# Performance work log

Measured on AMD Instinct MI355X. Metric: run time of the kernel, lower is better.

## Reference

```python
import jax, jax.numpy as jnp
import numpy as np

N, L, D = 256, 512, 512


def _attention(x, W_in, W_out, apply_tanh):
    # x: [N, L, D]; 'general' attention: project query, score against context (=x)
    q = jnp.einsum('bld,ed->ble', x, W_in)          # [N, L, D]
    scores = jnp.einsum('bld,bmd->blm', q, x)       # [N, L, L]
    w = jax.nn.softmax(scores, axis=-1)             # softmax over keys
    mix = jnp.einsum('blm,bmd->bld', w, x)          # [N, L, D]
    comb = jnp.concatenate([mix, q], axis=-1)       # [N, L, 2D]
    out = jnp.einsum('blc,dc->bld', comb, W_out)    # Linear(2D, D), no bias
    return jnp.tanh(out) if apply_tanh else out


def setup_inputs() -> dict:
    key = jax.random.key(0)
    k1, k2, k3, k4, k5 = jax.random.split(key, 5)
    s = 0.02
    return {
        'embeddings': jax.random.normal(k1, (N, L, D), dtype=jnp.float32),
        'W_in1': jax.random.normal(k2, (D, D), dtype=jnp.float32) * s,
        'W_out1': jax.random.normal(k3, (D, 2 * D), dtype=jnp.float32) * s,
        'W_in2': jax.random.normal(k4, (D, D), dtype=jnp.float32) * s,
        'W_out2': jax.random.normal(k5, (D, 2 * D), dtype=jnp.float32) * s,
    }


def reference(embeddings, W_in1, W_out1, W_in2, W_out2):
    x = _attention(embeddings, W_in1, W_out1, apply_tanh=True)   # block 1 (tanh)
    x = _attention(x, W_in2, W_out2, apply_tanh=False)           # block 2 (no tanh)
    # transpose(1,2) + avg_pool1d over full length == mean over L
    pooled = jnp.mean(x, axis=1)                                  # [N, D]
    return pooled.reshape(pooled.shape[0], -1, 1, 1)              # [N, D, 1, 1]
```

## Files before the change

### kernel.cpp

```cpp
#include <hip/hip_runtime.h>
#include <cstdint>
#include <cstddef>

typedef uint16_t u16;
typedef __attribute__((ext_vector_type(8))) short bf16x8;
typedef __attribute__((ext_vector_type(4))) float f32x4;
typedef __attribute__((ext_vector_type(4))) uint16_t u16x4;

#define GLOBAL_AS(p) (const __attribute__((address_space(1))) void*)(p)
#define LDS_AS(p)    (__attribute__((address_space(3))) void*)(p)

__device__ __forceinline__ void wait_all_bar(){
  asm volatile("s_waitcnt vmcnt(0) lgkmcnt(0)" ::: "memory");
  __builtin_amdgcn_s_barrier();
  asm volatile("" ::: "memory");
}
__device__ __forceinline__ void wait_lgkm_bar(){
  asm volatile("s_waitcnt lgkmcnt(0)" ::: "memory");
  __builtin_amdgcn_s_barrier();
  asm volatile("" ::: "memory");
}

__device__ __forceinline__ u16 f2b(float f){
  uint32_t u = __float_as_uint(f);
  u += 0x7fff + ((u >> 16) & 1);
  return (u16)(u >> 16);
}
__device__ __forceinline__ float b2f(u16 h){
  return __uint_as_float(((uint32_t)h) << 16);
}

__global__ void cvt_bf16_kernel(const float* __restrict__ src, u16* __restrict__ dst, int n){
  int i = (blockIdx.x * 256 + threadIdx.x) * 4;
  if (i >= n) return;
  float4 f = *(const float4*)(src + i);
  u16x4 o; o.x = f2b(f.x); o.y = f2b(f.y); o.z = f2b(f.z); o.w = f2b(f.w);
  *(u16x4*)(dst + i) = o;
}

__global__ void cvtT_kernel(const float* __restrict__ src, u16* __restrict__ x, u16* __restrict__ xT){
  __shared__ u16 tile[64][68];
  size_t b = blockIdx.y;
  int t = blockIdx.x;
  int r0 = (t >> 3) * 64, c0 = (t & 7) * 64;
  const float* s = src + b * 262144;
  u16* dx = x + b * 262144;
  u16* dT = xT + b * 262144;
  int tx = threadIdx.x & 63, ty = threadIdx.x >> 6;
  #pragma unroll
  for (int k = 0; k < 16; k++){
    int r = ty * 16 + k;
    u16 v = f2b(s[(size_t)(r0 + r) * 512 + c0 + tx]);
    dx[(size_t)(r0 + r) * 512 + c0 + tx] = v;
    tile[r][tx] = v;
  }
  __syncthreads();
  #pragma unroll
  for (int k = 0; k < 16; k++){
    int c = ty * 16 + k;
    dT[(size_t)(c0 + c) * 512 + r0 + tx] = tile[tx][c];
  }
}

__global__ void transpose512_kernel(const u16* __restrict__ src, u16* __restrict__ dst){
  __shared__ u16 tile[64][68];
  size_t b = blockIdx.y;
  int t = blockIdx.x;
  int r0 = (t >> 3) * 64, c0 = (t & 7) * 64;
  const u16* s = src + b * 262144;
  u16* d = dst + b * 262144;
  int tx = threadIdx.x & 63, ty = threadIdx.x >> 6;
  #pragma unroll
  for (int k = 0; k < 16; k++){
    int r = ty * 16 + k;
    tile[r][tx] = s[(size_t)(r0 + r) * 512 + c0 + tx];
  }
  __syncthreads();
  #pragma unroll
  for (int k = 0; k < 16; k++){
    int c = ty * 16 + k;
    d[(size_t)(c0 + c) * 512 + r0 + tx] = tile[tx][c];
  }
}

__global__ __launch_bounds__(512, 2) void attn_kernel(
    const u16* __restrict__ q, const u16* __restrict__ x, const u16* __restrict__ xT,
    u16* __restrict__ mix, int batPerXcd)
{
  __shared__ __align__(16) u16 U[64 * 520];
  __shared__ __align__(16) u16 Bx[2][512 * 32];
  __shared__ float stats[2][64][8];
  const int64_t E = 262144;
  int id = blockIdx.x;
  int tile = (id >> 3) & 7;
  int64_t bat = (int64_t)(id & 7) * batPerXcd + (id >> 6);
  q += bat * E; x += bat * E; xT += bat * E; mix += bat * E;
  int m0 = tile * 64;
  int tid = threadIdx.x, lane = tid & 63, w = tid >> 6;
  int fr = lane & 15, qd = lane >> 4, fq = qd * 8;

  auto stage = [&](const u16* __restrict__ src, int buf, int k0){
    #pragma unroll
    for (int s = 0; s < 4; s++){
      const u16* g = src + (size_t)(s * 128 + (tid >> 2)) * 512 + k0 + (tid & 3) * 8;
      __builtin_amdgcn_global_load_lds(GLOBAL_AS(g), LDS_AS(&Bx[buf][s * 4096 + tid * 8]), 16, 0, 0);
    }
  };

  stage(x, 0, 0);

  #pragma unroll
  for (int c = 0; c < 8; c++){
    int id2 = c * 512 + tid;
    int row = id2 >> 6, cb = id2 & 63;
    *(bf16x8*)&U[row * 520 + cb * 8] =
        *(const bf16x8*)(q + (size_t)(m0 + row) * 512 + cb * 8);
  }

  f32x4 acc[4][4];
  #pragma unroll
  for (int i = 0; i < 4; i++)
    #pragma unroll
    for (int j = 0; j < 4; j++) acc[i][j] = (f32x4){0.f, 0.f, 0.f, 0.f};

  wait_all_bar();

  for (int it = 0; it < 16; ++it){
    if (it < 15) stage(x, (it + 1) & 1, (it + 1) * 32);
    int k0 = it * 32;
    bf16x8 af[4], bfr[4];
    #pragma unroll
    for (int i = 0; i < 4; i++) af[i]  = *(const bf16x8*)&U[(i * 16 + fr) * 520 + k0 + fq];
    #pragma unroll
    for (int j = 0; j < 4; j++) bfr[j] = *(const bf16x8*)&Bx[it & 1][(w * 64 + j * 16 + fr) * 32 + fq];
    #pragma unroll
    for (int i = 0; i < 4; i++)
      #pragma unroll
      for (int j = 0; j < 4; j++)
        acc[i][j] = __builtin_amdgcn_mfma_f32_16x16x32_bf16(af[i], bfr[j], acc[i][j], 0, 0, 0);
    wait_all_bar();
  }

  stage(xT, 0, 0);

  float inv[4][4];
  #pragma unroll
  for (int i = 0; i < 4; i++)
    #pragma unroll
    for (int r = 0; r < 4; r++){
      float m = acc[i][0][r];
      #pragma unroll
      for (int j = 1; j < 4; j++) m = fmaxf(m, acc[i][j][r]);
      #pragma unroll
      for (int o = 1; o <= 8; o <<= 1) m = fmaxf(m, __shfl_xor(m, o));
      if (fr == 0) stats[0][i * 16 + qd * 4 + r][w] = m;
    }
  wait_lgkm_bar();
  #pragma unroll
  for (int i = 0; i < 4; i++)
    #pragma unroll
    for (int r = 0; r < 4; r++){
      int row = i * 16 + qd * 4 + r;
      float m = stats[0][row][0];
      #pragma unroll
      for (int t = 1; t < 8; t++) m = fmaxf(m, stats[0][row][t]);
      float s = 0.f;
      #pragma unroll
      for (int j = 0; j < 4; j++){
        float e = __expf(acc[i][j][r] - m);
        acc[i][j][r] = e; s += e;
      }
      #pragma unroll
      for (int o = 1; o <= 8; o <<= 1) s += __shfl_xor(s, o);
      if (fr == 0) stats[1][row][w] = s;
    }
  wait_lgkm_bar();
  #pragma unroll
  for (int i = 0; i < 4; i++)
    #pragma unroll
    for (int r = 0; r < 4; r++){
      int row = i * 16 + qd * 4 + r;
      float s = stats[1][row][0];
      #pragma unroll
      for (int t = 1; t < 8; t++) s += stats[1][row][t];
      inv[i][r] = 1.0f / s;
    }
  #pragma unroll
  for (int i = 0; i < 4; i++)
    #pragma unroll
    for (int r = 0; r < 4; r++)
      #pragma unroll
      for (int j = 0; j < 4; j++){
        int row = i * 16 + qd * 4 + r;
        int col = w * 64 + j * 16 + fr;
        uint32_t mine = f2b(acc[i][j][r] * inv[i][r]);
        uint32_t oth = (uint32_t)__shfl_xor((int)mine, 1);
        if (!(fr & 1)) *(uint32_t*)&U[row * 520 + col] = mine | (oth << 16);
      }
  wait_all_bar();

  #pragma unroll
  for (int i = 0; i < 4; i++)
    #pragma unroll
    for (int j = 0; j < 4; j++) acc[i][j] = (f32x4){0.f, 0.f, 0.f, 0.f};
  for (int it = 0; it < 16; ++it){
    if (it < 15) stage(xT, (it + 1) & 1, (it + 1) * 32);
    int k0 = it * 32;
    bf16x8 af[4], bfr[4];
    #pragma unroll
    for (int i = 0; i < 4; i++) af[i]  = *(const bf16x8*)&U[(i * 16 + fr) * 520 + k0 + fq];
    #pragma unroll
    for (int j = 0; j < 4; j++) bfr[j] = *(const bf16x8*)&Bx[it & 1][(w * 64 + j * 16 + fr) * 32 + fq];
    #pragma unroll
    for (int i = 0; i < 4; i++)
      #pragma unroll
      for (int j = 0; j < 4; j++)
        acc[i][j] = __builtin_amdgcn_mfma_f32_16x16x32_bf16(af[i], bfr[j], acc[i][j], 0, 0, 0);
    wait_all_bar();
  }
  #pragma unroll
  for (int i = 0; i < 4; i++)
    #pragma unroll
    for (int j = 0; j < 4; j++)
      #pragma unroll
      for (int r = 0; r < 4; r++)
        mix[(size_t)(m0 + i * 16 + qd * 4 + r) * 512 + w * 64 + j * 16 + fr] =
            f2b(acc[i][j][r]);
}

template<bool SPLIT, bool TANH, bool POOL, typename CT>
__global__ __launch_bounds__(256, 2) void gemm_bt_kernel(
    const u16* __restrict__ A0, const u16* __restrict__ A1,
    const u16* __restrict__ B, CT* __restrict__ C,
    int K, int ldb, int64_t aBatch, int64_t bBatch, int64_t cBatch,
    float* __restrict__ poolOut, int b0)
{
  __shared__ __align__(16) u16 As[2][128 * 32];
  __shared__ __align__(16) u16 Bs[2][128 * 32];
  int64_t bat = blockIdx.y;
  int m0 = (blockIdx.x & 3) * 128, n0 = (blockIdx.x >> 2) * 128;
  A0 += bat * aBatch;
  if (SPLIT) A1 += bat * aBatch;
  B += bat * bBatch;
  if (!POOL) C += bat * cBatch;
  int tid = threadIdx.x, lane = tid & 63;
  int w = tid >> 6;
  int wm = (w >> 1) * 64, wn = (w & 1) * 64;
  f32x4 acc[4][4];
  #pragma unroll
  for (int i = 0; i < 4; i++)
    #pragma unroll
    for (int j = 0; j < 4; j++) acc[i][j] = (f32x4){0.f, 0.f, 0.f, 0.f};

  int sRow = tid >> 2, sCol = (tid & 3) * 8;
  int fr = lane & 15, fq = (lane >> 4) * 8;

  auto stageG = [&](int buf, int k0){
    const u16* Ap = A0; int kk = k0;
    if (SPLIT && k0 >= 512){ Ap = A1; kk = k0 - 512; }
    const u16* ga = Ap + (size_t)(m0 + sRow) * 512 + kk + sCol;
    const u16* gb = B  + (size_t)(n0 + sRow) * ldb + k0 + sCol;
    __builtin_amdgcn_global_load_lds(GLOBAL_AS(ga),                    LDS_AS(&As[buf][tid * 8]),        16, 0, 0);
    __builtin_amdgcn_global_load_lds(GLOBAL_AS(ga + (size_t)64 * 512), LDS_AS(&As[buf][2048 + tid * 8]), 16, 0, 0);
    __builtin_amdgcn_global_load_lds(GLOBAL_AS(gb),                    LDS_AS(&Bs[buf][tid * 8]),        16, 0, 0);
    __builtin_amdgcn_global_load_lds(GLOBAL_AS(gb + (size_t)64 * ldb), LDS_AS(&Bs[buf][2048 + tid * 8]), 16, 0, 0);
  };

  stageG(0, 0);
  wait_all_bar();

  int nIt = K >> 5;
  for (int it = 0; it < nIt; ++it){
    if (it + 1 < nIt) stageG((it + 1) & 1, (it + 1) * 32);
    bf16x8 af[4], bfr[4];
    #pragma unroll
    for (int i = 0; i < 4; i++) af[i]  = *(const bf16x8*)&As[it & 1][(wm + i * 16 + fr) * 32 + fq];
    #pragma unroll
    for (int j = 0; j < 4; j++) bfr[j] = *(const bf16x8*)&Bs[it & 1][(wn + j * 16 + fr) * 32 + fq];
    #pragma unroll
    for (int i = 0; i < 4; i++)
      #pragma unroll
      for (int j = 0; j < 4; j++)
        acc[i][j] = __builtin_amdgcn_mfma_f32_16x16x32_bf16(af[i], bfr[j], acc[i][j], 0, 0, 0);
    wait_all_bar();
  }

  if constexpr (POOL){
    #pragma unroll
    for (int j = 0; j < 4; j++){
      float p = 0.f;
      #pragma unroll
      for (int i = 0; i < 4; i++)
        #pragma unroll
        for (int r = 0; r < 4; r++) p += acc[i][j][r];
      p += __shfl_xor(p, 16);
      p += __shfl_xor(p, 32);
      if (lane < 16){
        int col = n0 + wn + j * 16 + lane;
        atomicAdd(poolOut + ((size_t)(b0) + bat) * 512 + col, p * (1.0f / 512.0f));
      }
    }
  } else {
    int cq = (lane >> 4) * 4, cc = lane & 15;
    #pragma unroll
    for (int i = 0; i < 4; i++){
      #pragma unroll
      for (int j = 0; j < 4; j++){
        #pragma unroll
        for (int r = 0; r < 4; r++){
          int row = m0 + wm + i * 16 + cq + r;
          int col = n0 + wn + j * 16 + cc;
          float v = acc[i][j][r];
          if (TANH) v = tanhf(v);
          if constexpr (sizeof(CT) == 4) C[(size_t)row * 512 + col] = v;
          else                           C[(size_t)row * 512 + col] = f2b(v);
        }
      }
    }
  }
}

extern "C" void kernel_launch(void* const* d_in, const int* in_sizes, int n_in,
                              void* d_out, int out_size, void* d_ws, size_t ws_size,
                              hipStream_t stream) {
  const float* emb   = (const float*)d_in[0];
  const float* Win1  = (const float*)d_in[1];
  const float* Wout1 = (const float*)d_in[2];
  const float* Win2  = (const float*)d_in[3];
  const float* Wout2 = (const float*)d_in[4];
  float* out = (float*)d_out;

  int CB = 256;
  while (CB > 8 && (4ull << 20) + (size_t)CB * (5ull * 524288ull) > ws_size) CB >>= 1;
  const int64_t E = 262144;

  char* wsb = (char*)d_ws;
  u16* Win1b  = (u16*)wsb;
  u16* Wout1b = Win1b + 262144;
  u16* Win2b  = Wout1b + 524288;
  u16* Wout2b = Win2b + 262144;
  u16* base = (u16*)(wsb + (4 << 20));
  u16* Ar = base;
  u16* Br = base + (size_t)CB * E;
  u16* Cr = base + 2 * (size_t)CB * E;
  u16* Dr = base + 3 * (size_t)CB * E;
  u16* Fr = base + 4 * (size_t)CB * E;

  hipMemsetAsync(d_out, 0, (size_t)out_size * sizeof(float), stream);

  cvt_bf16_kernel<<<256, 256, 0, stream>>>(Win1,  Win1b,  262144);
  cvt_bf16_kernel<<<512, 256, 0, stream>>>(Wout1, Wout1b, 524288);
  cvt_bf16_kernel<<<256, 256, 0, stream>>>(Win2,  Win2b,  262144);
  cvt_bf16_kernel<<<512, 256, 0, stream>>>(Wout2, Wout2b, 524288);

  dim3 gg(16, CB);
  dim3 gt(64, CB);
  int nAttnBlocks = CB * 8;
  int batPerXcd = CB / 8;

  for (int c = 0; c < 256 / CB; c++){
    const float* embc = emb + (size_t)c * CB * 262144;
    int b0 = c * CB;

    cvtT_kernel<<<gt, 256, 0, stream>>>(embc, Ar, Cr);
    gemm_bt_kernel<false,false,false,u16><<<gg, 256, 0, stream>>>(
        Ar, nullptr, Win1b, Br, 512, 512, E, 0, E, nullptr, 0);
    attn_kernel<<<nAttnBlocks, 512, 0, stream>>>(Br, Ar, Cr, Fr, batPerXcd);
    gemm_bt_kernel<true,true,false,u16><<<gg, 256, 0, stream>>>(
        Fr, Br, Wout1b, Dr, 1024, 1024, E, 0, E, nullptr, 0);

    transpose512_kernel<<<gt, 256, 0, stream>>>(Dr, Cr);
    gemm_bt_kernel<false,false,false,u16><<<gg, 256, 0, stream>>>(
        Dr, nullptr, Win2b, Ar, 512, 512, E, 0, E, nullptr, 0);
    attn_kernel<<<nAttnBlocks, 512, 0, stream>>>(Ar, Dr, Cr, Fr, batPerXcd);
    gemm_bt_kernel<true,false,true,u16><<<gg, 256, 0, stream>>>(
        Fr, Ar, Wout2b, (u16*)nullptr, 1024, 1024, E, 0, 0, out, b0);
  }
}
```

Baseline: 1.754 ms.

## Shrink attention query tile to 32 rows and stream key fragments directly into registers

The attention kernel now processes 32 query rows per block instead of 64, doubling the grid. It drops the LDS double-buffered staging of x/xT tiles and the per-iteration barriers, loading B fragments straight from global memory into registers with a one-step register prefetch. The smaller LDS footprint and a launch bound of 4 blocks per SM are meant to raise occupancy and remove barrier stalls. In exchange, each block rereads the full x/xT from global or L2, doubling that traffic, and each B fragment now feeds only two MFMAs instead of four.

```diff
diff --git a/kernel.cpp b/kernel.cpp
--- a/kernel.cpp
+++ b/kernel.cpp
@@ -83,69 +83,65 @@
   }
 }
 
-__global__ __launch_bounds__(512, 2) void attn_kernel(
+__global__ __launch_bounds__(512, 4) void attn_kernel(
     const u16* __restrict__ q, const u16* __restrict__ x, const u16* __restrict__ xT,
     u16* __restrict__ mix, int batPerXcd)
 {
-  __shared__ __align__(16) u16 U[64 * 520];
-  __shared__ __align__(16) u16 Bx[2][512 * 32];
-  __shared__ float stats[2][64][8];
+  __shared__ __align__(16) u16 U[32 * 520];
+  __shared__ float stats[2][32][8];
   const int64_t E = 262144;
   int id = blockIdx.x;
-  int tile = (id >> 3) & 7;
-  int64_t bat = (int64_t)(id & 7) * batPerXcd + (id >> 6);
+  int tile = (id >> 3) & 15;
+  int64_t bat = (int64_t)(id & 7) * batPerXcd + (id >> 7);
   q += bat * E; x += bat * E; xT += bat * E; mix += bat * E;
-  int m0 = tile * 64;
+  int m0 = tile * 32;
   int tid = threadIdx.x, lane = tid & 63, w = tid >> 6;
   int fr = lane & 15, qd = lane >> 4, fq = qd * 8;
 
-  auto stage = [&](const u16* __restrict__ src, int buf, int k0){
-    #pragma unroll
-    for (int s = 0; s < 4; s++){
-      const u16* g = src + (size_t)(s * 128 + (tid >> 2)) * 512 + k0 + (tid & 3) * 8;
-      __builtin_amdgcn_global_load_lds(GLOBAL_AS(g), LDS_AS(&Bx[buf][s * 4096 + tid * 8]), 16, 0, 0);
-    }
-  };
-
-  stage(x, 0, 0);
-
-  #pragma unroll
-  for (int c = 0; c < 8; c++){
-    int id2 = c * 512 + tid;
-    int row = id2 >> 6, cb = id2 & 63;
-    *(bf16x8*)&U[row * 520 + cb * 8] =
-        *(const bf16x8*)(q + (size_t)(m0 + row) * 512 + cb * 8);
-  }
-
-  f32x4 acc[4][4];
-  #pragma unroll
-  for (int i = 0; i < 4; i++)
+  #pragma unroll
+  for (int c = 0; c < 4; c++){
+    int row = c * 8 + w;
+    __builtin_amdgcn_global_load_lds(GLOBAL_AS(q + (size_t)(m0 + row) * 512 + lane * 8),
+                                     LDS_AS(&U[row * 520 + lane * 8]), 16, 0, 0);
+  }
+  wait_all_bar();
+
+  int vo[4];
+  #pragma unroll
+  for (int j = 0; j < 4; j++) vo[j] = (w * 64 + j * 16 + fr) * 512 + fq;
+
+  f32x4 acc[2][4];
+  #pragma unroll
+  for (int i = 0; i < 2; i++)
     #pragma unroll
     for (int j = 0; j < 4; j++) acc[i][j] = (f32x4){0.f, 0.f, 0.f, 0.f};
 
-  wait_all_bar();
-
+  bf16x8 cur[4], nxt[4];
+  #pragma unroll
+  for (int j = 0; j < 4; j++) cur[j] = *(const bf16x8*)(x + vo[j]);
+  #pragma unroll
   for (int it = 0; it < 16; ++it){
-    if (it < 15) stage(x, (it + 1) & 1, (it + 1) * 32);
+    #pragma unroll
+    for (int j = 0; j < 4; j++)
+      if (it < 15) nxt[j] = *(const bf16x8*)(x + vo[j] + (it + 1) * 32);
     int k0 = it * 32;
-    bf16x8 af[4], bfr[4];
-    #pragma unroll
-    for (int i = 0; i < 4; i++) af[i]  = *(const bf16x8*)&U[(i * 16 + fr) * 520 + k0 + fq];
-    #pragma unroll
-    for (int j = 0; j < 4; j++) bfr[j] = *(const bf16x8*)&Bx[it & 1][(w * 64 + j * 16 + fr) * 32 + fq];
-    #pragma unroll
-    for (int i = 0; i < 4; i++)
-      #pragma unroll
-      for (int j = 0; j < 4; j++)
-        acc[i][j] = __builtin_amdgcn_mfma_f32_16x16x32_bf16(af[i], bfr[j], acc[i][j], 0, 0, 0);
-    wait_all_bar();
-  }
-
-  stage(xT, 0, 0);
-
-  float inv[4][4];
-  #pragma unroll
-  for (int i = 0; i < 4; i++)
+    bf16x8 a0 = *(const bf16x8*)&U[fr * 520 + k0 + fq];
+    bf16x8 a1 = *(const bf16x8*)&U[(16 + fr) * 520 + k0 + fq];
+    #pragma unroll
+    for (int j = 0; j < 4; j++){
+      acc[0][j] = __builtin_amdgcn_mfma_f32_16x16x32_bf16(a0, cur[j], acc[0][j], 0, 0, 0);
+      acc[1][j] = __builtin_amdgcn_mfma_f32_16x16x32_bf16(a1, cur[j], acc[1][j], 0, 0, 0);
+    }
+    #pragma unroll
+    for (int j = 0; j < 4; j++) cur[j] = nxt[j];
+  }
+
+  #pragma unroll
+  for (int j = 0; j < 4; j++) cur[j] = *(const bf16x8*)(xT + vo[j]);
+
+  float inv[2][4];
+  #pragma unroll
+  for (int i = 0; i < 2; i++)
     #pragma unroll
     for (int r = 0; r < 4; r++){
       float m = acc[i][0][r];
@@ -157,7 +153,7 @@
     }
   wait_lgkm_bar();
   #pragma unroll
-  for (int i = 0; i < 4; i++)
+  for (int i = 0; i < 2; i++)
     #pragma unroll
     for (int r = 0; r < 4; r++){
       int row = i * 16 + qd * 4 + r;
@@ -176,7 +172,7 @@
     }
   wait_lgkm_bar();
   #pragma unroll
-  for (int i = 0; i < 4; i++)
+  for (int i = 0; i < 2; i++)
     #pragma unroll
     for (int r = 0; r < 4; r++){
       int row = i * 16 + qd * 4 + r;
@@ -186,7 +182,7 @@
       inv[i][r] = 1.0f / s;
     }
   #pragma unroll
-  for (int i = 0; i < 4; i++)
+  for (int i = 0; i < 2; i++)
     #pragma unroll
     for (int r = 0; r < 4; r++)
       #pragma unroll
@@ -197,29 +193,30 @@
         uint32_t oth = (uint32_t)__shfl_xor((int)mine, 1);
         if (!(fr & 1)) *(uint32_t*)&U[row * 520 + col] = mine | (oth << 16);
       }
-  wait_all_bar();
-
-  #pragma unroll
-  for (int i = 0; i < 4; i++)
+  wait_lgkm_bar();
+
+  #pragma unroll
+  for (int i = 0; i < 2; i++)
     #pragma unroll
     for (int j = 0; j < 4; j++) acc[i][j] = (f32x4){0.f, 0.f, 0.f, 0.f};
+  #pragma unroll
   for (int it = 0; it < 16; ++it){
-    if (it < 15) stage(xT, (it + 1) & 1, (it + 1) * 32);
+    #pragma unroll
+    for (int j = 0; j < 4; j++)
+      if (it < 15) nxt[j] = *(const bf16x8*)(xT + vo[j] + (it + 1) * 32);
     int k0 = it * 32;
-    bf16x8 af[4], bfr[4];
-    #pragma unroll
-    for (int i = 0; i < 4; i++) af[i]  = *(const bf16x8*)&U[(i * 16 + fr) * 520 + k0 + fq];
-    #pragma unroll
-    for (int j = 0; j < 4; j++) bfr[j] = *(const bf16x8*)&Bx[it & 1][(w * 64 + j * 16 + fr) * 32 + fq];
-    #pragma unroll
-    for (int i = 0; i < 4; i++)
-      #pragma unroll
-      for (int j = 0; j < 4; j++)
-        acc[i][j] = __builtin_amdgcn_mfma_f32_16x16x32_bf16(af[i], bfr[j], acc[i][j], 0, 0, 0);
-    wait_all_bar();
-  }
-  #pragma unroll
-  for (int i = 0; i < 4; i++)
+    bf16x8 a0 = *(const bf16x8*)&U[fr * 520 + k0 + fq];
+    bf16x8 a1 = *(const bf16x8*)&U[(16 + fr) * 520 + k0 + fq];
+    #pragma unroll
+    for (int j = 0; j < 4; j++){
+      acc[0][j] = __builtin_amdgcn_mfma_f32_16x16x32_bf16(a0, cur[j], acc[0][j], 0, 0, 0);
+      acc[1][j] = __builtin_amdgcn_mfma_f32_16x16x32_bf16(a1, cur[j], acc[1][j], 0, 0, 0);
+    }
+    #pragma unroll
+    for (int j = 0; j < 4; j++) cur[j] = nxt[j];
+  }
+  #pragma unroll
+  for (int i = 0; i < 2; i++)
     #pragma unroll
     for (int j = 0; j < 4; j++)
       #pragma unroll
@@ -355,7 +352,7 @@
 
   dim3 gg(16, CB);
   dim3 gt(64, CB);
-  int nAttnBlocks = CB * 8;
+  int nAttnBlocks = CB * 16;
   int batPerXcd = CB / 8;
 
   for (int c = 0; c < 256 / CB; c++){
```

New measurement: 2.042 ms. 16.4% more time.

## Swizzle LDS tiles and overlap next-stage loads with partial vmcnt waits

Applied to the files above, without the earlier changes.

Both the attention and GEMM kernels now issue the next tile's global-to-LDS loads before waiting. They wait with vmcnt(4) so only the current tile must have landed, instead of draining all loads at the end of each iteration. The staged column offset is XOR-swizzled by row, with matching read offsets, to cut LDS bank conflicts on fragment reads. The q tile load now goes through global_load_lds, and the xT prefetch is folded into the last iteration of the first loop. The partial-count waits rely on exact per-thread load ordering, and any mismatch in counts or swizzle would corrupt the results.

```diff
diff --git a/kernel.cpp b/kernel.cpp
--- a/kernel.cpp
+++ b/kernel.cpp
@@ -10,12 +10,22 @@
 #define GLOBAL_AS(p) (const __attribute__((address_space(1))) void*)(p)
 #define LDS_AS(p)    (__attribute__((address_space(3))) void*)(p)
 
-__device__ __forceinline__ void wait_all_bar(){
-  asm volatile("s_waitcnt vmcnt(0) lgkmcnt(0)" ::: "memory");
+__device__ __forceinline__ void bar_vm4(){
+  asm volatile("s_waitcnt vmcnt(4)" ::: "memory");
   __builtin_amdgcn_s_barrier();
   asm volatile("" ::: "memory");
 }
-__device__ __forceinline__ void wait_lgkm_bar(){
+__device__ __forceinline__ void bar_vm0(){
+  asm volatile("s_waitcnt vmcnt(0)" ::: "memory");
+  __builtin_amdgcn_s_barrier();
+  asm volatile("" ::: "memory");
+}
+__device__ __forceinline__ void bar_end(){
+  asm volatile("" ::: "memory");
+  __builtin_amdgcn_s_barrier();
+  asm volatile("" ::: "memory");
+}
+__device__ __forceinline__ void bar_lgkm(){
   asm volatile("s_waitcnt lgkmcnt(0)" ::: "memory");
   __builtin_amdgcn_s_barrier();
   asm volatile("" ::: "memory");
@@ -25,9 +35,6 @@
   uint32_t u = __float_as_uint(f);
   u += 0x7fff + ((u >> 16) & 1);
   return (u16)(u >> 16);
-}
-__device__ __forceinline__ float b2f(u16 h){
-  return __uint_as_float(((uint32_t)h) << 16);
 }
 
 __global__ void cvt_bf16_kernel(const float* __restrict__ src, u16* __restrict__ dst, int n){
@@ -97,12 +104,15 @@
   q += bat * E; x += bat * E; xT += bat * E; mix += bat * E;
   int m0 = tile * 64;
   int tid = threadIdx.x, lane = tid & 63, w = tid >> 6;
-  int fr = lane & 15, qd = lane >> 4, fq = qd * 8;
+  int fr = lane & 15, qd = lane >> 4;
+  int fq = qd * 8;
+  int sw = ((tid & 3) ^ ((tid >> 3) & 3)) * 8;
+  int bslot = (qd ^ ((fr >> 1) & 3)) * 8;
 
   auto stage = [&](const u16* __restrict__ src, int buf, int k0){
     #pragma unroll
     for (int s = 0; s < 4; s++){
-      const u16* g = src + (size_t)(s * 128 + (tid >> 2)) * 512 + k0 + (tid & 3) * 8;
+      const u16* g = src + (size_t)(s * 128 + (tid >> 2)) * 512 + k0 + sw;
       __builtin_amdgcn_global_load_lds(GLOBAL_AS(g), LDS_AS(&Bx[buf][s * 4096 + tid * 8]), 16, 0, 0);
     }
   };
@@ -111,10 +121,9 @@
 
   #pragma unroll
   for (int c = 0; c < 8; c++){
-    int id2 = c * 512 + tid;
-    int row = id2 >> 6, cb = id2 & 63;
-    *(bf16x8*)&U[row * 520 + cb * 8] =
-        *(const bf16x8*)(q + (size_t)(m0 + row) * 512 + cb * 8);
+    int row = c * 8 + w;
+    __builtin_amdgcn_global_load_lds(GLOBAL_AS(q + (size_t)(m0 + row) * 512 + lane * 8),
+                                     LDS_AS(&U[row * 520 + lane * 8]), 16, 0, 0);
   }
 
   f32x4 acc[4][4];
@@ -122,26 +131,24 @@
   for (int i = 0; i < 4; i++)
     #pragma unroll
     for (int j = 0; j < 4; j++) acc[i][j] = (f32x4){0.f, 0.f, 0.f, 0.f};
-
-  wait_all_bar();
 
   for (int it = 0; it < 16; ++it){
     if (it < 15) stage(x, (it + 1) & 1, (it + 1) * 32);
+    else         stage(xT, 0, 0);
+    bar_vm4();
     int k0 = it * 32;
     bf16x8 af[4], bfr[4];
     #pragma unroll
     for (int i = 0; i < 4; i++) af[i]  = *(const bf16x8*)&U[(i * 16 + fr) * 520 + k0 + fq];
     #pragma unroll
-    for (int j = 0; j < 4; j++) bfr[j] = *(const bf16x8*)&Bx[it & 1][(w * 64 + j * 16 + fr) * 32 + fq];
+    for (int j = 0; j < 4; j++) bfr[j] = *(const bf16x8*)&Bx[it & 1][(w * 64 + j * 16 + fr) * 32 + bslot];
     #pragma unroll
     for (int i = 0; i < 4; i++)
       #pragma unroll
       for (int j = 0; j < 4; j++)
         acc[i][j] = __builtin_amdgcn_mfma_f32_16x16x32_bf16(af[i], bfr[j], acc[i][j], 0, 0, 0);
-    wait_all_bar();
-  }
-
-  stage(xT, 0, 0);
+    bar_end();
+  }
 
   float inv[4][4];
   #pragma unroll
@@ -155,7 +162,7 @@
       for (int o = 1; o <= 8; o <<= 1) m = fmaxf(m, __shfl_xor(m, o));
       if (fr == 0) stats[0][i * 16 + qd * 4 + r][w] = m;
     }
-  wait_lgkm_bar();
+  bar_lgkm();
   #pragma unroll
   for (int i = 0; i < 4; i++)
     #pragma unroll
@@ -174,7 +181,7 @@
       for (int o = 1; o <= 8; o <<= 1) s += __shfl_xor(s, o);
       if (fr == 0) stats[1][row][w] = s;
     }
-  wait_lgkm_bar();
+  bar_lgkm();
   #pragma unroll
   for (int i = 0; i < 4; i++)
     #pragma unroll
@@ -197,26 +204,27 @@
         uint32_t oth = (uint32_t)__shfl_xor((int)mine, 1);
         if (!(fr & 1)) *(uint32_t*)&U[row * 520 + col] = mine | (oth << 16);
       }
-  wait_all_bar();
+  bar_lgkm();
 
   #pragma unroll
   for (int i = 0; i < 4; i++)
     #pragma unroll
     for (int j = 0; j < 4; j++) acc[i][j] = (f32x4){0.f, 0.f, 0.f, 0.f};
   for (int it = 0; it < 16; ++it){
-    if (it < 15) stage(xT, (it + 1) & 1, (it + 1) * 32);
+    if (it < 15){ stage(xT, (it + 1) & 1, (it + 1) * 32); bar_vm4(); }
+    else        { bar_vm0(); }
     int k0 = it * 32;
     bf16x8 af[4], bfr[4];
     #pragma unroll
     for (int i = 0; i < 4; i++) af[i]  = *(const bf16x8*)&U[(i * 16 + fr) * 520 + k0 + fq];
     #pragma unroll
-    for (int j = 0; j < 4; j++) bfr[j] = *(const bf16x8*)&Bx[it & 1][(w * 64 + j * 16 + fr) * 32 + fq];
+    for (int j = 0; j < 4; j++) bfr[j] = *(const bf16x8*)&Bx[it & 1][(w * 64 + j * 16 + fr) * 32 + bslot];
     #pragma unroll
     for (int i = 0; i < 4; i++)
       #pragma unroll
       for (int j = 0; j < 4; j++)
         acc[i][j] = __builtin_amdgcn_mfma_f32_16x16x32_bf16(af[i], bfr[j], acc[i][j], 0, 0, 0);
-    wait_all_bar();
+    bar_end();
   }
   #pragma unroll
   for (int i = 0; i < 4; i++)
@@ -252,8 +260,10 @@
     #pragma unroll
     for (int j = 0; j < 4; j++) acc[i][j] = (f32x4){0.f, 0.f, 0.f, 0.f};
 
-  int sRow = tid >> 2, sCol = (tid & 3) * 8;
-  int fr = lane & 15, fq = (lane >> 4) * 8;
+  int sRow = tid >> 2;
+  int sCol = ((tid & 3) ^ ((tid >> 3) & 3)) * 8;
+  int fr = lane & 15;
+  int fq = ((lane >> 4) ^ ((fr >> 1) & 3)) * 8;
 
   auto stageG = [&](int buf, int k0){
     const u16* Ap = A0; int kk = k0;
@@ -267,11 +277,11 @@
   };
 
   stageG(0, 0);
-  wait_all_bar();
 
   int nIt = K >> 5;
   for (int it = 0; it < nIt; ++it){
-    if (it + 1 < nIt) stageG((it + 1) & 1, (it + 1) * 32);
+    if (it + 1 < nIt){ stageG((it + 1) & 1, (it + 1) * 32); bar_vm4(); }
+    else             { bar_vm0(); }
     bf16x8 af[4], bfr[4];
     #pragma unroll
     for (int i = 0; i < 4; i++) af[i]  = *(const bf16x8*)&As[it & 1][(wm + i * 16 + fr) * 32 + fq];
@@ -282,7 +292,7 @@
       #pragma unroll
       for (int j = 0; j < 4; j++)
         acc[i][j] = __builtin_amdgcn_mfma_f32_16x16x32_bf16(af[i], bfr[j], acc[i][j], 0, 0, 0);
-    wait_all_bar();
+    bar_end();
   }
 
   if constexpr (POOL){
```

Result: faster. 1.709 ms (-2.6%).
